# Kernel optimization log

Hardware: AMD Instinct MI355X
Metric: run time of the kernel (lower is better)

Reference implementation:

```python
import jax, jax.numpy as jnp
import numpy as np

EPS = 1e-5

def _conv1x1_bn_relu(x, w, b, g, beta, m, v):
    # x: [B,C,H,W], w: [O,C] (1x1 conv), inference-mode BatchNorm, ReLU
    y = jnp.einsum('bchw,oc->bohw', x, w) + b[None, :, None, None]
    scale = (g / jnp.sqrt(v + EPS))[None, :, None, None]
    shift = (beta - m * g / jnp.sqrt(v + EPS))[None, :, None, None]
    return jax.nn.relu(y * scale + shift)

def _maxpool3s2p1(x):
    # MaxPool2d(kernel_size=3, stride=2, padding=1) on NCHW
    return jax.lax.reduce_window(x, -jnp.inf, jax.lax.max,
                                 (1, 1, 3, 3), (1, 1, 2, 2),
                                 ((0, 0), (0, 0), (1, 1), (1, 1)))

def setup_inputs() -> dict:
    key = jax.random.key(0)
    ks = jax.random.split(key, 24)
    B, C, H, W = 8, 256, 64, 64
    C2 = C // 2
    d = {}
    d['a'] = jax.random.normal(ks[0], (B, C, H, W), dtype=jnp.float32)
    d['conv1_w'] = jax.random.normal(ks[1], (C2, C), dtype=jnp.float32) * 0.05
    d['conv1_b'] = jax.random.normal(ks[2], (C2,), dtype=jnp.float32) * 0.05
    d['bn1_g'] = jax.random.uniform(ks[3], (C2,), dtype=jnp.float32, minval=0.5, maxval=1.5)
    d['bn1_b'] = jax.random.normal(ks[4], (C2,), dtype=jnp.float32) * 0.05
    d['bn1_m'] = jax.random.normal(ks[5], (C2,), dtype=jnp.float32) * 0.05
    d['bn1_v'] = jax.random.uniform(ks[6], (C2,), dtype=jnp.float32, minval=0.5, maxval=1.5)
    d['conv2_w'] = jax.random.normal(ks[7], (C2, C), dtype=jnp.float32) * 0.05
    d['conv2_b'] = jax.random.normal(ks[8], (C2,), dtype=jnp.float32) * 0.05
    d['bn2_g'] = jax.random.uniform(ks[9], (C2,), dtype=jnp.float32, minval=0.5, maxval=1.5)
    d['bn2_b'] = jax.random.normal(ks[10], (C2,), dtype=jnp.float32) * 0.05
    d['bn2_m'] = jax.random.normal(ks[11], (C2,), dtype=jnp.float32) * 0.05
    d['bn2_v'] = jax.random.uniform(ks[12], (C2,), dtype=jnp.float32, minval=0.5, maxval=1.5)
    d['conv3_w'] = jax.random.normal(ks[13], (C, C2), dtype=jnp.float32) * 0.05
    d['conv3_b'] = jax.random.normal(ks[14], (C,), dtype=jnp.float32) * 0.05
    d['bn3_g'] = jax.random.uniform(ks[15], (C,), dtype=jnp.float32, minval=0.5, maxval=1.5)
    d['bn3_b'] = jax.random.normal(ks[16], (C,), dtype=jnp.float32) * 0.05
    d['bn3_m'] = jax.random.normal(ks[17], (C,), dtype=jnp.float32) * 0.05
    d['bn3_v'] = jax.random.uniform(ks[18], (C,), dtype=jnp.float32, minval=0.5, maxval=1.5)
    return d

def reference(a, conv1_w, conv1_b, bn1_g, bn1_b, bn1_m, bn1_v,
              conv2_w, conv2_b, bn2_g, bn2_b, bn2_m, bn2_v,
              conv3_w, conv3_b, bn3_g, bn3_b, bn3_m, bn3_v):
    B, C, H, W = a.shape
    # branch 1: conv1x1+BN+ReLU, raw reshape [B, H*W, C/2] (flat order, as torch.reshape)
    x1 = _conv1x1_bn_relu(a, conv1_w, conv1_b, bn1_g, bn1_b, bn1_m, bn1_v)
    C2 = x1.shape[1]
    x1 = x1.reshape(B, -1, C2)  # [B, HW, C2] via raw flatten (NOT a transpose)
    # branch 2/3: conv1x1+BN+ReLU+maxpool; torch calls self.conv2 twice with same weights
    x23 = _maxpool3s2p1(_conv1x1_bn_relu(a, conv2_w, conv2_b, bn2_g, bn2_b, bn2_m, bn2_v))
    x2 = x23.reshape(B, C2, -1)   # [B, C2, HW/4]
    x3 = x23.reshape(B, -1, C2)   # [B, HW/4, C2] raw flatten
    # non-local attention: softmax(x1 @ x2) @ x3
    attn = jax.nn.softmax(jnp.matmul(x1, x2), axis=2)  # [B, HW, HW/4]
    out = jnp.matmul(attn, x3)                          # [B, HW, C2]
    out = out.reshape(B, C2, H, W)                      # raw reshape back to NCHW
    out = _conv1x1_bn_relu(out, conv3_w, conv3_b, bn3_g, bn3_b, bn3_m, bn3_v)
    return out + a
```

## Files before the change

kernel.cpp:

```cpp
#include <hip/hip_runtime.h>
#include <hip/hip_bf16.h>


typedef unsigned short u16;
typedef unsigned int u32;
typedef short  bf16x8 __attribute__((ext_vector_type(8)));
typedef float  f32x4  __attribute__((ext_vector_type(4)));

#define DEV static __device__ __forceinline__

DEV float bf2f(u16 v){ return __uint_as_float(((u32)v)<<16); }
DEV float bflo(u32 p){ return __uint_as_float(p<<16); }
DEV float bfhi(u32 p){ return __uint_as_float(p & 0xFFFF0000u); }
DEV u16 f2bf(float f){
  u32 x = __float_as_uint(f);
  x += 0x7FFFu + ((x>>16)&1u);
  return (u16)(x>>16);
}
DEV u32 pack2(float a, float b){ return ((u32)f2bf(a)) | (((u32)f2bf(b))<<16); }

__global__ __launch_bounds__(256) void k_t1(const float* __restrict__ a, u16* __restrict__ aTg){
  __shared__ u16 L[64*72];
  const int t = threadIdx.x;
  const int hw0 = blockIdx.x*64, c0 = blockIdx.y*64, b = blockIdx.z;
  const float* ab = a + b*1048576;
  #pragma unroll
  for(int it=0; it<4; ++it){
    int c = it*16 + (t>>4);
    int hw = (t&15)*4;
    float4 f = *(const float4*)&ab[(c0+c)*4096 + hw0 + hw];
    L[(hw+0)*72 + c] = f2bf(f.x);
    L[(hw+1)*72 + c] = f2bf(f.y);
    L[(hw+2)*72 + c] = f2bf(f.z);
    L[(hw+3)*72 + c] = f2bf(f.w);
  }
  __syncthreads();
  u16* ob = aTg + b*1048576;
  #pragma unroll
  for(int it=0; it<2; ++it){
    int g2 = it*256 + t;
    int hw = g2>>3, k = g2&7;
    *(uint4*)&ob[(hw0+hw)*256 + c0 + k*8] = *(const uint4*)&L[hw*72 + k*8];
  }
}

__global__ __launch_bounds__(256) void k_t2(const u16* __restrict__ y1, u16* __restrict__ x4T){
  __shared__ u16 L[64*72];
  const int t = threadIdx.x;
  const int hw0 = blockIdx.x*64, c20 = blockIdx.y*64, b = blockIdx.z;
  const u16* yb = y1 + b*524288;
  #pragma unroll
  for(int it=0; it<2; ++it){
    int c2 = it*32 + (t>>3);
    int hw = (t&7)*8;
    uint4 d = *(const uint4*)&yb[(c20+c2)*4096 + hw0 + hw];
    const u16* dv = (const u16*)&d;
    #pragma unroll
    for(int j=0;j<8;j++) L[(hw+j)*72 + c2] = dv[j];
  }
  __syncthreads();
  u16* ob = x4T + b*524288;
  #pragma unroll
  for(int it=0; it<2; ++it){
    int g2 = it*256 + t;
    int hw = g2>>3, k = g2&7;
    *(uint4*)&ob[(hw0+hw)*128 + c20 + k*8] = *(const uint4*)&L[hw*72 + k*8];
  }
}

__global__ __launch_bounds__(512) void k_conv12m(
    const u16* __restrict__ aTg, const float* __restrict__ w1, const float* __restrict__ w2,
    const float* __restrict__ b1, const float* __restrict__ g1, const float* __restrict__ be1,
    const float* __restrict__ m1, const float* __restrict__ v1,
    const float* __restrict__ b2, const float* __restrict__ g2, const float* __restrict__ be2,
    const float* __restrict__ m2, const float* __restrict__ v2,
    u16* __restrict__ y1, u16* __restrict__ y2)
{
  __shared__ __align__(16) u16 aL[128*64];
  __shared__ __align__(16) u16 wL[256*64];
  __shared__ float scL[256], shL[256];
  const int tid = threadIdx.x;
  const int wv = tid>>6, l = tid&63, g = l>>4, q = l&15;
  const int wpx = wv>>2, woc = wv&3;
  const int px0 = blockIdx.x*128, b = blockIdx.y;

  if (tid < 256){
    int oc = tid, cv = oc>>7, j = oc&127;
    float bias = cv? b2[j] : b1[j];
    float gg   = cv? g2[j] : g1[j];
    float be   = cv? be2[j]: be1[j];
    float mm   = cv? m2[j] : m1[j];
    float vv   = cv? v2[j] : v1[j];
    float sc = gg / sqrtf(vv + 1e-5f);
    scL[oc] = sc;
    shL[oc] = (bias - mm)*sc + be;
  }

  const u16* aTb = aTg + b*1048576;
  const int spx = tid>>2, su = (tid&3)*2;
  uint4 areg[2]; float4 wreg[8];
  {
    areg[0] = *(const uint4*)&aTb[(px0+spx)*256 + 0*64 + su*8];
    areg[1] = *(const uint4*)&aTb[(px0+spx)*256 + 0*64 + (su+1)*8];
    #pragma unroll
    for(int it=0; it<8; ++it){
      int ocr = it*32 + (tid>>4); int fu = tid&15;
      const float* wp = (it<4)? &w1[ocr*256] : &w2[(ocr-128)*256];
      wreg[it] = *(const float4*)&wp[0*64 + fu*4];
    }
  }

  f32x4 acc[4][4];
  #pragma unroll
  for(int m=0;m<4;m++){
    #pragma unroll
    for(int n=0;n<4;n++) acc[m][n] = (f32x4){0.f,0.f,0.f,0.f};
  }

  for(int kc=0; kc<4; ++kc){
    __syncthreads();
    *(uint4*)((char*)aL + spx*128 + (( su   ^(spx&7))<<4)) = areg[0];
    *(uint4*)((char*)aL + spx*128 + (((su+1)^(spx&7))<<4)) = areg[1];
    #pragma unroll
    for(int it=0; it<8; ++it){
      int ocr = it*32 + (tid>>4), fu = tid&15, u = fu>>1, h = fu&1;
      *(uint2*)((char*)wL + ocr*128 + ((u^(ocr&7))<<4) + h*8)
          = make_uint2(pack2(wreg[it].x, wreg[it].y), pack2(wreg[it].z, wreg[it].w));
    }
    __syncthreads();
    if (kc<3){
      areg[0] = *(const uint4*)&aTb[(px0+spx)*256 + (kc+1)*64 + su*8];
      areg[1] = *(const uint4*)&aTb[(px0+spx)*256 + (kc+1)*64 + (su+1)*8];
      #pragma unroll
      for(int it=0; it<8; ++it){
        int ocr = it*32 + (tid>>4); int fu = tid&15;
        const float* wp = (it<4)? &w1[ocr*256] : &w2[(ocr-128)*256];
        wreg[it] = *(const float4*)&wp[(kc+1)*64 + fu*4];
      }
    }
    #pragma unroll
    for(int ks=0; ks<2; ++ks){
      bf16x8 Af[4], Bf[4];
      #pragma unroll
      for(int n=0;n<4;n++)
        Af[n] = *(const bf16x8*)((char*)wL + (woc*64+n*16+q)*128 + (((ks*4+g)^(q&7))<<4));
      #pragma unroll
      for(int m=0;m<4;m++)
        Bf[m] = *(const bf16x8*)((char*)aL + (wpx*64+m*16+q)*128 + (((ks*4+g)^(q&7))<<4));
      #pragma unroll
      for(int m=0;m<4;m++){
        #pragma unroll
        for(int n=0;n<4;n++)
          acc[m][n] = __builtin_amdgcn_mfma_f32_16x16x32_bf16(Af[n], Bf[m], acc[m][n], 0,0,0);
      }
    }
  }

  u16* yb   = (woc < 2) ? (y1 + b*524288) : (y2 + b*524288);
  const int coff = (woc < 2) ? 0 : 128;
  #pragma unroll
  for(int m=0;m<4;m++){
    int px = px0 + wpx*64 + m*16 + q;
    #pragma unroll
    for(int n=0;n<4;n++){
      #pragma unroll
      for(int e=0;e<4;e++){
        int oc = woc*64 + n*16 + g*4 + e;
        yb[(oc - coff)*4096 + px] = f2bf(fmaxf(acc[m][n][e]*scL[oc] + shL[oc], 0.f));
      }
    }
  }
}

__global__ __launch_bounds__(256) void k_pool(const u16* __restrict__ y2,
                                              u16* __restrict__ pTg, u16* __restrict__ x3Tg){
  int idx = blockIdx.x*256 + threadIdx.x;
  int b = idx>>17, rem = idx & 131071;
  int c = rem>>10, pos = rem&1023;
  int oh = pos>>5, ow = pos&31;
  const u16* base = y2 + b*524288 + c*4096;
  float mx = -1e30f;
  #pragma unroll
  for(int dh=-1; dh<=1; ++dh){
    int ih = 2*oh+dh;
    if ((unsigned)ih < 64u){
      #pragma unroll
      for(int dw=-1; dw<=1; ++dw){
        int iw = 2*ow+dw;
        if((unsigned)iw<64u) mx = fmaxf(mx, bf2f(base[ih*64+iw]));
      }
    }
  }
  u16 v = f2bf(mx);
  pTg[b*131072 + pos*128 + c] = v;
  int f = c*1024 + pos;
  x3Tg[b*131072 + (f&127)*1024 + (f>>7)] = v;
}

__global__ __launch_bounds__(256) void k_attn_mfma(u16* __restrict__ y1,
    const u16* __restrict__ pTg, const u16* __restrict__ x3Tg)
{
  __shared__ __align__(16) u16 qT[64*128];
  __shared__ __align__(16) u16 kT[64*128];
  __shared__ __align__(16) u16 vT[128*64];
  __shared__ __align__(16) u16 pS[4][1024];

  const int tid = threadIdx.x, w = tid>>6, l = tid&63;
  const int g = l>>4, q = l&15;
  const int b = blockIdx.y;
  const int R0 = blockIdx.x*64;
  u16* y1b = y1 + b*524288;
  const u16* pTb = pTg + b*131072;
  const u16* vTb = x3Tg + b*131072;

  #pragma unroll
  for (int it=0; it<4; ++it){
    int idx = it*256 + tid;
    int row = idx>>4, c16 = idx&15;
    uint4 d = *(const uint4*)(y1b + (R0+row)*128 + c16*8);
    *(uint4*)((char*)qT + row*256 + ((c16 ^ (row&15))<<4)) = d;
  }
  __syncthreads();

  bf16x8 qf[4];
  #pragma unroll
  for (int kk=0; kk<4; ++kk)
    qf[kk] = *(const bf16x8*)((char*)qT + (w*16+q)*256 + (((kk*4+g) ^ q)<<4));

  f32x4 O[8];
  #pragma unroll
  for (int t=0;t<8;t++) O[t] = (f32x4){0.f,0.f,0.f,0.f};
  float m = -3.0e38f, s = 0.f;

  for (int ch=0; ch<16; ++ch){
    const int kv0 = ch*64;
    uint4 kreg[4], vreg[4];
    #pragma unroll
    for (int it=0; it<4; ++it){
      int idx = it*256 + tid;
      kreg[it] = *(const uint4*)(pTb + (kv0 + (idx>>4))*128 + (idx&15)*8);
      vreg[it] = *(const uint4*)(vTb + (idx>>3)*1024 + kv0 + (idx&7)*8);
    }
    __syncthreads();
    #pragma unroll
    for (int it=0; it<4; ++it){
      int idx = it*256 + tid;
      int row = idx>>4, c16 = idx&15;
      *(uint4*)((char*)kT + row*256 + ((c16 ^ (row&15))<<4)) = kreg[it];
      int vr = idx>>3, vc = idx&7;
      *(uint4*)((char*)vT + vr*128 + ((vc ^ (vr&7))<<4)) = vreg[it];
    }
    __syncthreads();

    f32x4 st[4];
    #pragma unroll
    for (int n=0;n<4;n++) st[n] = (f32x4){0.f,0.f,0.f,0.f};
    #pragma unroll
    for (int kk=0; kk<4; ++kk){
      #pragma unroll
      for (int n=0;n<4;n++){
        bf16x8 kf = *(const bf16x8*)((char*)kT + (n*16+q)*256 + (((kk*4+g) ^ q)<<4));
        st[n] = __builtin_amdgcn_mfma_f32_16x16x32_bf16(kf, qf[kk], st[n], 0,0,0);
      }
    }

    float cmax = st[0][0];
    #pragma unroll
    for(int n=0;n<4;n++){
      #pragma unroll
      for(int e=0;e<4;e++) cmax = fmaxf(cmax, st[n][e]);
    }
    cmax = fmaxf(cmax, __shfl_xor(cmax,16,64));
    cmax = fmaxf(cmax, __shfl_xor(cmax,32,64));
    float mnew = fmaxf(m, cmax);
    float corr = __expf(m - mnew);
    m = mnew;
    float psum = 0.f;
    #pragma unroll
    for(int n=0;n<4;n++){
      #pragma unroll
      for(int e=0;e<4;e++){ float t_ = __expf(st[n][e]-m); st[n][e]=t_; psum += t_; }
    }
    psum += __shfl_xor(psum,16,64);
    psum += __shfl_xor(psum,32,64);
    s = s*corr + psum;

    float cO[4];
    #pragma unroll
    for(int e=0;e<4;e++) cO[e] = __shfl(corr, g*4+e, 64);
    #pragma unroll
    for(int t=0;t<8;t++){
      #pragma unroll
      for(int e=0;e<4;e++) O[t][e] *= cO[e];
    }

    u16* pSw = pS[w];
    #pragma unroll
    for(int n=0;n<4;n++){
      u32 lo = pack2(st[n][0], st[n][1]);
      u32 hi = pack2(st[n][2], st[n][3]);
      *(uint2*)((char*)pSw + q*128 + (((n*4+g) ^ q)<<3)) = make_uint2(lo,hi);
    }

    #pragma unroll
    for(int kk2=0; kk2<2; ++kk2){
      int kv4a = kk2*8 + g*2;
      uint2 A0 = *(const uint2*)((char*)pSw + q*128 + (((kv4a  ) ^ q)<<3));
      uint2 A1 = *(const uint2*)((char*)pSw + q*128 + (((kv4a+1) ^ q)<<3));
      uint4 pa4 = make_uint4(A0.x, A0.y, A1.x, A1.y);
      bf16x8 pf = *(bf16x8*)&pa4;
      #pragma unroll
      for(int t=0;t<8;t++){
        bf16x8 vf = *(const bf16x8*)((char*)vT + (t*16+q)*128 + (((kk2*4+g) ^ (q&7))<<4));
        O[t] = __builtin_amdgcn_mfma_f32_16x16x32_bf16(pf, vf, O[t], 0,0,0);
      }
    }
  }

  float si[4];
  #pragma unroll
  for(int e=0;e<4;e++) si[e] = 1.0f / __shfl(s, g*4+e, 64);
  u16* ob = y1b + R0*128;
  #pragma unroll
  for(int t=0;t<8;t++){
    #pragma unroll
    for(int e=0;e<4;e++){
      int grow = w*16 + g*4 + e;
      ob[grow*128 + t*16 + q] = f2bf(O[t][e]*si[e]);
    }
  }
}

__global__ __launch_bounds__(512) void k_conv3m(
    const u16* __restrict__ x4T, const float* __restrict__ w3,
    const float* __restrict__ b3, const float* __restrict__ g3, const float* __restrict__ be3,
    const float* __restrict__ m3, const float* __restrict__ v3,
    const float* __restrict__ a,  float* __restrict__ out)
{
  __shared__ __align__(16) u16 xL[128*64];
  __shared__ __align__(16) u16 wL[256*64];
  __shared__ float scL[256], shL[256];
  const int tid = threadIdx.x;
  const int wv = tid>>6, l = tid&63, g = l>>4, q = l&15;
  const int wpx = wv>>2, woc = wv&3;
  const int hw0 = blockIdx.x*128, b = blockIdx.y;

  if (tid < 256){
    int oc = tid;
    float sc = g3[oc] / sqrtf(v3[oc] + 1e-5f);
    scL[oc] = sc;
    shL[oc] = (b3[oc] - m3[oc])*sc + be3[oc];
  }

  const u16* xb = x4T + b*524288;
  const int shw = tid>>2, su = (tid&3)*2;
  uint4 xreg[2]; float4 wreg[8];
  {
    xreg[0] = *(const uint4*)&xb[(hw0+shw)*128 + 0*64 + su*8];
    xreg[1] = *(const uint4*)&xb[(hw0+shw)*128 + 0*64 + (su+1)*8];
    #pragma unroll
    for(int it=0; it<8; ++it){
      int ocr = it*32 + (tid>>4); int fu = tid&15;
      wreg[it] = *(const float4*)&w3[ocr*128 + 0*64 + fu*4];
    }
  }

  f32x4 acc[4][4];
  #pragma unroll
  for(int m=0;m<4;m++){
    #pragma unroll
    for(int n=0;n<4;n++) acc[m][n] = (f32x4){0.f,0.f,0.f,0.f};
  }

  for(int kc=0; kc<2; ++kc){
    __syncthreads();
    *(uint4*)((char*)xL + shw*128 + (( su   ^(shw&7))<<4)) = xreg[0];
    *(uint4*)((char*)xL + shw*128 + (((su+1)^(shw&7))<<4)) = xreg[1];
    #pragma unroll
    for(int it=0; it<8; ++it){
      int ocr = it*32 + (tid>>4), fu = tid&15, u = fu>>1, h = fu&1;
      *(uint2*)((char*)wL + ocr*128 + ((u^(ocr&7))<<4) + h*8)
          = make_uint2(pack2(wreg[it].x, wreg[it].y), pack2(wreg[it].z, wreg[it].w));
    }
    __syncthreads();
    if (kc<1){
      xreg[0] = *(const uint4*)&xb[(hw0+shw)*128 + 64 + su*8];
      xreg[1] = *(const uint4*)&xb[(hw0+shw)*128 + 64 + (su+1)*8];
      #pragma unroll
      for(int it=0; it<8; ++it){
        int ocr = it*32 + (tid>>4); int fu = tid&15;
        wreg[it] = *(const float4*)&w3[ocr*128 + 64 + fu*4];
      }
    }
    #pragma unroll
    for(int ks=0; ks<2; ++ks){
      bf16x8 Af[4], Bf[4];
      #pragma unroll
      for(int n=0;n<4;n++)
        Af[n] = *(const bf16x8*)((char*)wL + (woc*64+n*16+q)*128 + (((ks*4+g)^(q&7))<<4));
      #pragma unroll
      for(int m=0;m<4;m++)
        Bf[m] = *(const bf16x8*)((char*)xL + (wpx*64+m*16+q)*128 + (((ks*4+g)^(q&7))<<4));
      #pragma unroll
      for(int m=0;m<4;m++){
        #pragma unroll
        for(int n=0;n<4;n++)
          acc[m][n] = __builtin_amdgcn_mfma_f32_16x16x32_bf16(Af[n], Bf[m], acc[m][n], 0,0,0);
      }
    }
  }

  const float* ab = a + b*1048576;
  float* ob = out + b*1048576;
  #pragma unroll
  for(int m=0;m<4;m++){
    int hw = hw0 + wpx*64 + m*16 + q;
    #pragma unroll
    for(int n=0;n<4;n++){
      #pragma unroll
      for(int e=0;e<4;e++){
        int oc = woc*64 + n*16 + g*4 + e;
        int gi = oc*4096 + hw;
        ob[gi] = fmaxf(acc[m][n][e]*scL[oc] + shL[oc], 0.f) + ab[gi];
      }
    }
  }
}

extern "C" void kernel_launch(void* const* d_in, const int* in_sizes, int n_in,
                              void* d_out, int out_size, void* d_ws, size_t ws_size,
                              hipStream_t stream)
{
  const float* a   = (const float*)d_in[0];
  const float* w1  = (const float*)d_in[1];
  const float* b1  = (const float*)d_in[2];
  const float* g1  = (const float*)d_in[3];
  const float* be1 = (const float*)d_in[4];
  const float* m1  = (const float*)d_in[5];
  const float* v1  = (const float*)d_in[6];
  const float* w2  = (const float*)d_in[7];
  const float* b2  = (const float*)d_in[8];
  const float* g2  = (const float*)d_in[9];
  const float* be2 = (const float*)d_in[10];
  const float* m2  = (const float*)d_in[11];
  const float* v2  = (const float*)d_in[12];
  const float* w3  = (const float*)d_in[13];
  const float* b3  = (const float*)d_in[14];
  const float* g3  = (const float*)d_in[15];
  const float* be3 = (const float*)d_in[16];
  const float* m3  = (const float*)d_in[17];
  const float* v3  = (const float*)d_in[18];
  float* out = (float*)d_out;

  u16* d16  = (u16*)d_out;
  u16* aTg  = d16;
  u16* pT   = d16;
  u16* x3T  = d16 + 1048576;
  u16* y2   = d16 + 8388608;
  u16* y1   = d16 + 12582912;
  u16* x4T  = (u16*)d_ws;

  k_t1      <<<dim3(64,4,8), 256, 0, stream>>>(a, aTg);
  k_conv12m <<<dim3(32,8),   512, 0, stream>>>(aTg,w1,w2,b1,g1,be1,m1,v1,b2,g2,be2,m2,v2,y1,y2);
  k_pool    <<<dim3(4096),   256, 0, stream>>>(y2, pT, x3T);
  k_attn_mfma<<<dim3(64,8),  256, 0, stream>>>(y1, pT, x3T);
  k_t2      <<<dim3(64,2,8), 256, 0, stream>>>(y1, x4T);
  k_conv3m  <<<dim3(32,8),   512, 0, stream>>>(x4T,w3,b3,g3,be3,m3,v3,a,out);
}
```

Baseline: 249.3 us.

## Load attention Q/K/V fragments directly from global memory instead of LDS staging

Removes the shared-memory staging of Q, K and V tiles in the flash-style attention kernel, together with the two block-wide barriers per KV chunk. MFMA operand fragments are now read straight from global memory, relying on L1/L2 caching because all four waves read the same K/V data. This cuts LDS traffic and synchronization and frees LDS for occupancy. The cost is redundant global/cache loads per wave, strided V reads, and exposed global latency with no explicit prefetching.

```diff
diff --git a/kernel.cpp b/kernel.cpp
--- a/kernel.cpp
+++ b/kernel.cpp
@@ -200,9 +200,6 @@
 __global__ __launch_bounds__(256) void k_attn_mfma(u16* __restrict__ y1,
     const u16* __restrict__ pTg, const u16* __restrict__ x3Tg)
 {
-  __shared__ __align__(16) u16 qT[64*128];
-  __shared__ __align__(16) u16 kT[64*128];
-  __shared__ __align__(16) u16 vT[128*64];
   __shared__ __align__(16) u16 pS[4][1024];
 
   const int tid = threadIdx.x, w = tid>>6, l = tid&63;
@@ -213,19 +210,10 @@
   const u16* pTb = pTg + b*131072;
   const u16* vTb = x3Tg + b*131072;
 
-  #pragma unroll
-  for (int it=0; it<4; ++it){
-    int idx = it*256 + tid;
-    int row = idx>>4, c16 = idx&15;
-    uint4 d = *(const uint4*)(y1b + (R0+row)*128 + c16*8);
-    *(uint4*)((char*)qT + row*256 + ((c16 ^ (row&15))<<4)) = d;
-  }
-  __syncthreads();
-
   bf16x8 qf[4];
   #pragma unroll
   for (int kk=0; kk<4; ++kk)
-    qf[kk] = *(const bf16x8*)((char*)qT + (w*16+q)*256 + (((kk*4+g) ^ q)<<4));
+    qf[kk] = *(const bf16x8*)&y1b[(R0 + w*16 + q)*128 + (kk*4+g)*8];
 
   f32x4 O[8];
   #pragma unroll
@@ -234,34 +222,19 @@
 
   for (int ch=0; ch<16; ++ch){
     const int kv0 = ch*64;
-    uint4 kreg[4], vreg[4];
-    #pragma unroll
-    for (int it=0; it<4; ++it){
-      int idx = it*256 + tid;
-      kreg[it] = *(const uint4*)(pTb + (kv0 + (idx>>4))*128 + (idx&15)*8);
-      vreg[it] = *(const uint4*)(vTb + (idx>>3)*1024 + kv0 + (idx&7)*8);
-    }
-    __syncthreads();
-    #pragma unroll
-    for (int it=0; it<4; ++it){
-      int idx = it*256 + tid;
-      int row = idx>>4, c16 = idx&15;
-      *(uint4*)((char*)kT + row*256 + ((c16 ^ (row&15))<<4)) = kreg[it];
-      int vr = idx>>3, vc = idx&7;
-      *(uint4*)((char*)vT + vr*128 + ((vc ^ (vr&7))<<4)) = vreg[it];
-    }
-    __syncthreads();
 
     f32x4 st[4];
     #pragma unroll
     for (int n=0;n<4;n++) st[n] = (f32x4){0.f,0.f,0.f,0.f};
     #pragma unroll
     for (int kk=0; kk<4; ++kk){
-      #pragma unroll
-      for (int n=0;n<4;n++){
-        bf16x8 kf = *(const bf16x8*)((char*)kT + (n*16+q)*256 + (((kk*4+g) ^ q)<<4));
-        st[n] = __builtin_amdgcn_mfma_f32_16x16x32_bf16(kf, qf[kk], st[n], 0,0,0);
-      }
+      bf16x8 kf[4];
+      #pragma unroll
+      for (int n=0;n<4;n++)
+        kf[n] = *(const bf16x8*)&pTb[(kv0 + n*16 + q)*128 + (kk*4+g)*8];
+      #pragma unroll
+      for (int n=0;n<4;n++)
+        st[n] = __builtin_amdgcn_mfma_f32_16x16x32_bf16(kf[n], qf[kk], st[n], 0,0,0);
     }
 
     float cmax = st[0][0];
@@ -305,13 +278,13 @@
     #pragma unroll
     for(int kk2=0; kk2<2; ++kk2){
       int kv4a = kk2*8 + g*2;
-      uint2 A0 = *(const uint2*)((char*)pSw + q*128 + (((kv4a  ) ^ q)<<3));
-      uint2 A1 = *(const uint2*)((char*)pSw + q*128 + (((kv4a+1) ^ q)<<3));
+      uint2 A0 = *(const uint2*)((char*)pS[w] + q*128 + (((kv4a  ) ^ q)<<3));
+      uint2 A1 = *(const uint2*)((char*)pS[w] + q*128 + (((kv4a+1) ^ q)<<3));
       uint4 pa4 = make_uint4(A0.x, A0.y, A1.x, A1.y);
       bf16x8 pf = *(bf16x8*)&pa4;
       #pragma unroll
       for(int t=0;t<8;t++){
-        bf16x8 vf = *(const bf16x8*)((char*)vT + (t*16+q)*128 + (((kk2*4+g) ^ (q&7))<<4));
+        bf16x8 vf = *(const bf16x8*)&vTb[(t*16 + q)*1024 + kv0 + (kk2*4+g)*8];
         O[t] = __builtin_amdgcn_mfma_f32_16x16x32_bf16(pf, vf, O[t], 0,0,0);
       }
     }
```

Result: slower. 296.4 us (+18.9%).
